# Kernel optimization log

Hardware: AMD Instinct MI355X
Metric: run time of the kernel (lower is better)

Reference implementation:

```python
import jax, jax.numpy as jnp
import numpy as np

N, E, F_IN, F_E, H, HEADS, NG = 50000, 300000, 16, 8, 64, 4, 64
D_HEAD = H // HEADS
EPS = 1e-5


def setup_inputs() -> dict:
    key = jax.random.key(0)
    ks = jax.random.split(key, 12)
    def rn(k, shape, s=0.1):
        return jax.random.normal(k, shape, jnp.float32) * s
    return dict(
        x=jax.random.normal(ks[0], (N, F_IN), jnp.float32),
        edge_index=jax.random.randint(ks[1], (2, E), 0, N),
        edge_attr=jax.random.normal(ks[2], (E, F_E), jnp.float32),
        batch=jnp.sort(jax.random.randint(ks[3], (N,), 0, NG)),
        # edge_net: Linear(F_E, H*F_IN) -> ReLU -> Linear(H*F_IN, H*F_IN)
        en_w1=rn(ks[4], (F_E, H * F_IN)), en_b1=jnp.zeros((H * F_IN,), jnp.float32),
        en_w2=rn(ks[5], (H * F_IN, H * F_IN)), en_b2=jnp.zeros((H * F_IN,), jnp.float32),
        # NNConv root weight + bias
        root_w=rn(ks[6], (F_IN, H)), conv1_b=jnp.zeros((H,), jnp.float32),
        norm1_w=jnp.ones((H,), jnp.float32), norm1_b=jnp.zeros((H,), jnp.float32),
        # GATConv: lin weight, attention vectors, bias
        gat_w=rn(ks[7], (H, H)),
        att_src=rn(ks[8], (HEADS, D_HEAD)), att_dst=rn(ks[9], (HEADS, D_HEAD)),
        gat_b=jnp.zeros((H,), jnp.float32),
        norm2_w=jnp.ones((H,), jnp.float32), norm2_b=jnp.zeros((H,), jnp.float32),
        lin_w=rn(ks[10], (H, 1)), lin_b=jnp.zeros((1,), jnp.float32),
    )


def _graph_layernorm(x, w, b):
    # PyG LayerNorm(mode='graph') with batch=None: scalar mean/std over ALL elems
    mu = x.mean()
    sd = jnp.sqrt(((x - mu) ** 2).mean())
    return (x - mu) / (sd + EPS) * w + b


def reference(x, edge_index, edge_attr, batch, en_w1, en_b1, en_w2, en_b2,
              root_w, conv1_b, norm1_w, norm1_b, gat_w, att_src, att_dst,
              gat_b, norm2_w, norm2_b, lin_w, lin_b):
    src, dst = edge_index[0], edge_index[1]
    # --- NNConv: per-edge weight matrices from edge_net ---
    w_e = jax.nn.relu(edge_attr @ en_w1 + en_b1) @ en_w2 + en_b2
    w_e = w_e.reshape(E, F_IN, H)                      # [E, in, out]
    msg = jnp.einsum('ef,efh->eh', x[src], w_e)        # gather-matmul per edge
    agg = jax.ops.segment_sum(msg, dst, num_segments=N)
    deg = jax.ops.segment_sum(jnp.ones((E,), x.dtype), dst, num_segments=N)
    agg = agg / jnp.maximum(deg, 1.0)[:, None]         # aggr='mean'
    h = x @ root_w + agg + conv1_b
    h = jax.nn.relu(h)
    h = _graph_layernorm(h, norm1_w, norm1_b)
    # dropout: eval mode -> identity
    # --- GATConv (edge_attr=None at call site; add self-loops, softmax attn) ---
    loops = jnp.arange(N)
    s2 = jnp.concatenate([src, loops])
    d2 = jnp.concatenate([dst, loops])
    xh = (h @ gat_w).reshape(N, HEADS, D_HEAD)
    a_src = (xh * att_src).sum(-1)                     # [N, HEADS]
    a_dst = (xh * att_dst).sum(-1)
    alpha = jax.nn.leaky_relu(a_src[s2] + a_dst[d2], 0.2)  # [E+N, HEADS]
    amax = jax.ops.segment_max(alpha, d2, num_segments=N)
    alpha = jnp.exp(alpha - amax[d2])
    asum = jax.ops.segment_sum(alpha, d2, num_segments=N)
    alpha = alpha / (asum[d2] + 1e-16)
    out = jax.ops.segment_sum(alpha[:, :, None] * xh[s2], d2, num_segments=N)
    h2 = out.reshape(N, H) + gat_b                     # concat heads
    h2 = jax.nn.relu(h2)
    h2 = _graph_layernorm(h2, norm2_w, norm2_b)
    # --- global mean pool + linear head ---
    gs = jax.ops.segment_sum(h2, batch, num_segments=NG)
    cnt = jax.ops.segment_sum(jnp.ones((N,), h2.dtype), batch, num_segments=NG)
    pooled = gs / jnp.maximum(cnt, 1.0)[:, None]
    return pooled @ lin_w + lin_b                      # [NG, 1]
```

## Files before the change

kernel.cpp:

```cpp
#include <hip/hip_runtime.h>
#include <hip/hip_bf16.h>

#define N_NODES 50000
#define E_EDGES 300000
#define NGRAPH 64
#define NCHUNK 129
#define CSPLIT 65
#define NKG 1034
#define NEGRP 1172
#define LNEPS 1e-5f
#define NBLK_N 196
#define NBLK_P 12500
#define RPRE16 1.00048828125f

typedef _Float16 f16x8 __attribute__((ext_vector_type(8)));
typedef _Float16 f16x2 __attribute__((ext_vector_type(2)));
typedef float floatx16 __attribute__((ext_vector_type(16)));
typedef float f32x2 __attribute__((ext_vector_type(2)));
typedef unsigned int u32x4 __attribute__((ext_vector_type(4)));

__global__ void k_prep(const float* __restrict__ w2, const float* __restrict__ b2,
                       _Float16* __restrict__ Tt3) {
  __shared__ float tile[32][65];
  int t = threadIdx.x;
  int kg0 = blockIdx.x * 2;
  int kf0 = kg0 * 16;
  int kfr = t >> 6;
  int n0 = t & 63;
#pragma unroll
  for (int it = 0; it < 8; ++it) {
    int kfl = it * 4 + kfr;
    int kf = kf0 + kfl;
    float v = 0.f;
    if (kf < 16384) v = w2[(size_t)kf * 64 + n0];
    else if (kf < 16400) v = b2[(size_t)(kf - 16384) * 64 + n0];
    tile[kfl][n0] = v;
  }
  __syncthreads();
  int kgl = t >> 7;
  int half = (t >> 6) & 1;
  int n = t & 63;
  f16x8 pack;
#pragma unroll
  for (int j = 0; j < 8; ++j) pack[j] = (_Float16)tile[kgl * 16 + half * 8 + j][n];
  *(f16x8*)(Tt3 + (size_t)(kg0 + kgl) * 1024 + half * 512 + n * 8) = pack;
}

__global__ void k_prepw(const float* __restrict__ w1, float* __restrict__ W1t) {
  int i = blockIdx.x * 256 + threadIdx.x;
  if (i < 8192) { int k = i >> 3, j = i & 7; W1t[i] = w1[j * 1024 + k]; }
}

__global__ void k_cnt(const int* __restrict__ ei, int* __restrict__ degI) {
  int e = blockIdx.x * 256 + threadIdx.x;
  if (e < E_EDGES) atomicAdd(&degI[ei[E_EDGES + e]], 1);
}

__global__ void k_scanA(const int* __restrict__ degI, int* __restrict__ bsum) {
  __shared__ int sm[256];
  int t = threadIdx.x;
  int i = blockIdx.x * 256 + t;
  sm[t] = (i < N_NODES) ? degI[i] : 0;
  __syncthreads();
  for (int off = 128; off > 0; off >>= 1) {
    if (t < off) sm[t] += sm[t + off];
    __syncthreads();
  }
  if (t == 0) bsum[blockIdx.x] = sm[0];
}

__global__ void k_scanB(const int* __restrict__ bsum, int* __restrict__ bpre) {
  __shared__ int s[256];
  int t = threadIdx.x;
  int v = (t < NBLK_N) ? bsum[t] : 0;
  s[t] = v;
  __syncthreads();
  for (int off = 1; off < 256; off <<= 1) {
    int add = (t >= off) ? s[t - off] : 0;
    __syncthreads();
    s[t] += add;
    __syncthreads();
  }
  if (t < NBLK_N) bpre[t] = s[t] - v;
}

__global__ void k_scanC(const int* __restrict__ degI, const int* __restrict__ bpre,
                        int* __restrict__ rowptr, int* __restrict__ cursor) {
  __shared__ int s[256];
  int t = threadIdx.x;
  int i = blockIdx.x * 256 + t;
  int d = (i < N_NODES) ? degI[i] : 0;
  s[t] = d;
  __syncthreads();
  for (int off = 1; off < 256; off <<= 1) {
    int add = (t >= off) ? s[t - off] : 0;
    __syncthreads();
    s[t] += add;
    __syncthreads();
  }
  int r = bpre[blockIdx.x] + s[t] - d;
  if (i < N_NODES) {
    rowptr[i] = r;
    cursor[i] = r;
    if (i == N_NODES - 1) rowptr[N_NODES] = r + d;
  }
}

__global__ void k_scatter(const int* __restrict__ ei, int* __restrict__ cursor,
                          int* __restrict__ colsrc) {
  int e = blockIdx.x * 256 + threadIdx.x;
  if (e < E_EDGES) {
    int s = ei[e], d = ei[E_EDGES + e];
    int pos = atomicAdd(&cursor[d], 1);
    colsrc[pos] = s;
  }
}

__global__ __launch_bounds__(256, 4)
void k_nnconv(const float* __restrict__ x, const int* __restrict__ ei,
              const float* __restrict__ ea, const float* __restrict__ W1t,
              const float* __restrict__ b1, const _Float16* __restrict__ Tt3,
              float* __restrict__ agg) {
  const int tid = threadIdx.x;
  const int lane = tid & 63;
  const int l31 = lane & 31;
  const int half = lane >> 5;
  const int grp = blockIdx.x >> 1;
  const int piece = blockIdx.x & 1;
  const int cstart = piece ? CSPLIT : 0;
  const int cend = piece ? NCHUNK : CSPLIT;

  int e = grp * 256 + tid;
  bool valid = e < E_EDGES;
  int srcv = valid ? ei[e] : 0;
  int dstv = valid ? ei[E_EDGES + e] : -1;

  f32x2 ea2[4];
  {
    const float4* p = (const float4*)(ea + (size_t)(valid ? e : 0) * 8);
    float4 a0 = p[0], a1 = p[1];
    ea2[0] = (f32x2){a0.x, a0.y};
    ea2[1] = (f32x2){a0.z, a0.w};
    ea2[2] = (f32x2){a1.x, a1.y};
    ea2[3] = (f32x2){a1.z, a1.w};
  }

  const int f0 = half * 8;
  unsigned xh16[2][4];
#pragma unroll
  for (int mt = 0; mt < 2; ++mt) {
    int s = __shfl(srcv, mt * 32 + l31);
    const float4* px = (const float4*)(x + (size_t)s * 16 + f0);
    float4 v0 = px[0], v1 = px[1];
    xh16[mt][0] = __builtin_bit_cast(unsigned, __builtin_amdgcn_cvt_pkrtz(v0.x * RPRE16, v0.y * RPRE16));
    xh16[mt][1] = __builtin_bit_cast(unsigned, __builtin_amdgcn_cvt_pkrtz(v0.z * RPRE16, v0.w * RPRE16));
    xh16[mt][2] = __builtin_bit_cast(unsigned, __builtin_amdgcn_cvt_pkrtz(v1.x * RPRE16, v1.y * RPRE16));
    xh16[mt][3] = __builtin_bit_cast(unsigned, __builtin_amdgcn_cvt_pkrtz(v1.z * RPRE16, v1.w * RPRE16));
  }

  int bpaddr[2];
#pragma unroll
  for (int mt = 0; mt < 2; ++mt) bpaddr[mt] = (mt * 32 + l31) * 4;

  const _Float16* sb = Tt3 + (size_t)(cstart * 8) * 1024;
  const int loff = half * 512 + l31 * 8;

  f16x8 Bs[4][2];
  auto loadB = [&](int slot) {
    Bs[slot][0] = *(const f16x8*)(sb + loff);
    Bs[slot][1] = *(const f16x8*)(sb + loff + 256);
    sb += 1024;
  };

  unsigned prr[4];
  auto calcR = [&](int c, const float* w1p, const float* b1p) {
    if (c < 128) {
#pragma unroll
      for (int p = 0; p < 4; ++p) {
        float rv[2];
#pragma unroll
        for (int kk = 0; kk < 2; ++kk) {
          const f32x2* w = (const f32x2*)(w1p + (p * 2 + kk) * 8);
          f32x2 s01 = ea2[0] * w[0] + ea2[1] * w[1];
          f32x2 s23 = ea2[2] * w[2] + ea2[3] * w[3];
          f32x2 s = s01 + s23;
          rv[kk] = fmaxf(b1p[p * 2 + kk] + s[0] + s[1], 0.f) * RPRE16;
        }
        prr[p] = __builtin_bit_cast(unsigned, __builtin_amdgcn_cvt_pkrtz(rv[0], rv[1]));
      }
    } else {
      prr[0] = 0x00003C00u;
      prr[1] = prr[2] = prr[3] = 0u;
    }
  };

  unsigned ubuf[8];
  auto bcastR = [&]() {
#pragma unroll
    for (int p = 0; p < 4; ++p)
#pragma unroll
      for (int mt = 0; mt < 2; ++mt)
        ubuf[p * 2 + mt] = (unsigned)__builtin_amdgcn_ds_bpermute(bpaddr[mt], (int)prr[p]);
  };

  floatx16 acc[2][2];
#pragma unroll
  for (int mt = 0; mt < 2; ++mt)
#pragma unroll
    for (int nt = 0; nt < 2; ++nt)
#pragma unroll
      for (int r = 0; r < 16; ++r) acc[mt][nt][r] = 0.f;

  calcR(cstart, W1t + cstart * 64, b1 + cstart * 8);
  bcastR();
  loadB(0);
  loadB(1);
  const float* w1p = W1t + (cstart + 1) * 64;
  const float* b1p = b1 + (cstart + 1) * 8;

  for (int c = cstart; c < cend; ++c) {
    unsigned rsp[16];
#pragma unroll
    for (int p = 0; p < 4; ++p)
#pragma unroll
      for (int mt = 0; mt < 2; ++mt) {
        unsigned u = ubuf[p * 2 + mt];
        rsp[(2 * p) * 2 + mt]     = __builtin_amdgcn_perm(u, 0u, 0x05040504u);
        rsp[(2 * p + 1) * 2 + mt] = __builtin_amdgcn_perm(u, 0u, 0x07060706u);
      }
    if (c + 1 < cend) {
      calcR(c + 1, w1p, b1p);
      bcastR();
      w1p += 64; b1p += 8;
    }
#pragma unroll
    for (int kg = 0; kg < 8; ++kg) {
      loadB((kg + 2) & 3);
#pragma unroll
      for (int mt = 0; mt < 2; ++mt) {
        f16x2 r2 = __builtin_bit_cast(f16x2, rsp[kg * 2 + mt]);
        u32x4 U;
#pragma unroll
        for (int j = 0; j < 4; ++j)
          U[j] = __builtin_bit_cast(unsigned,
                   __builtin_bit_cast(f16x2, xh16[mt][j]) * r2);
        f16x8 A = __builtin_bit_cast(f16x8, U);
#pragma unroll
        for (int nt = 0; nt < 2; ++nt)
          acc[mt][nt] = __builtin_amdgcn_mfma_f32_32x32x16_f16(A, Bs[kg & 3][nt], acc[mt][nt], 0, 0, 0);
      }
    }
  }

#pragma unroll
  for (int mt = 0; mt < 2; ++mt) {
#pragma unroll
    for (int reg = 0; reg < 16; ++reg) {
      int el = mt * 32 + (reg & 3) + 8 * (reg >> 2) + 4 * half;
      int dd = __shfl(dstv, el);
      if (dd >= 0) {
#pragma unroll
        for (int nt = 0; nt < 2; ++nt)
          atomicAdd(&agg[(size_t)dd * 64 + nt * 32 + l31], acc[mt][nt][reg]);
      }
    }
  }
}

__global__ void k_root(const float* __restrict__ x, const float* __restrict__ rootw,
                       const float* __restrict__ conv1b, const float* __restrict__ agg,
                       const int* __restrict__ degI, float* __restrict__ hpre,
                       float* __restrict__ rpart) {
  __shared__ float sW[1024];
  __shared__ float sx[64];
  __shared__ float red[8];
  int t = threadIdx.x;
  int blk = blockIdx.x;
#pragma unroll
  for (int i = 0; i < 4; ++i) sW[t + i * 256] = rootw[t + i * 256];
  if (t < 64) sx[t] = x[(size_t)blk * 64 + t];
  __syncthreads();
  int ln = t >> 6, h = t & 63;
  int n = blk * 4 + ln;
  float acc = conv1b[h];
#pragma unroll
  for (int f = 0; f < 16; ++f) acc += sx[ln * 16 + f] * sW[f * 64 + h];
  float dv = fmaxf((float)degI[n], 1.0f);
  float v = acc + agg[(size_t)n * 64 + h] / dv;
  v = fmaxf(v, 0.f);
  hpre[(size_t)n * 64 + h] = v;
  float s1 = v, s2 = v * v;
  for (int o = 32; o > 0; o >>= 1) { s1 += __shfl_down(s1, o); s2 += __shfl_down(s2, o); }
  if ((t & 63) == 0) { red[t >> 6] = s1; red[4 + (t >> 6)] = s2; }
  __syncthreads();
  if (t == 0) {
    rpart[blk * 2] = red[0] + red[1] + red[2] + red[3];
    rpart[blk * 2 + 1] = red[4] + red[5] + red[6] + red[7];
  }
}

__global__ void k_fold1(const float* __restrict__ rpart, const float* __restrict__ n1w,
                        const float* __restrict__ n1b, const float* __restrict__ gatw,
                        float* __restrict__ gw2, float* __restrict__ tb) {
  __shared__ float red[8];
  __shared__ float sMI[2];
  __shared__ float sS[64], sT[64];
  int t = threadIdx.x;
  int wv = t >> 6, lane = t & 63;
  float a = 0.f, b = 0.f;
  for (int i = t; i < NBLK_P; i += 256) { a += rpart[2 * i]; b += rpart[2 * i + 1]; }
  for (int o = 32; o > 0; o >>= 1) { a += __shfl_down(a, o); b += __shfl_down(b, o); }
  if (lane == 0) { red[wv] = a; red[4 + wv] = b; }
  __syncthreads();
  if (t == 0) {
    float A = red[0] + red[1] + red[2] + red[3];
    float B = red[4] + red[5] + red[6] + red[7];
    const float M = (float)N_NODES * 64.f;
    float mu = A / M;
    float var = fmaxf(B / M - mu * mu, 0.f);
    sMI[0] = mu;
    sMI[1] = 1.f / (sqrtf(var) + LNEPS);
  }
  __syncthreads();
  if (t < 64) {
    float mu = sMI[0], inv = sMI[1];
    sS[t] = inv * n1w[t];
    sT[t] = n1b[t] - mu * inv * n1w[t];
  }
  __syncthreads();
  if (t < 64) {
    float acc = 0.f;
    for (int i = 0; i < 64; ++i) {
      float g = gatw[i * 64 + t];
      gw2[i * 64 + t] = sS[i] * g;
      acc += sT[i] * g;
    }
    tb[t] = acc;
  }
}

__global__ void k_gatlin(const float* __restrict__ hpre, const float* __restrict__ gw2,
                         const float* __restrict__ tb, const float* __restrict__ attS,
                         const float* __restrict__ attD, float* __restrict__ xh,
                         float* __restrict__ asrc, float* __restrict__ adst) {
  __shared__ float sW[4096];
  __shared__ float sh[256];
  __shared__ float sxh[256];
  int t = threadIdx.x;
  int blk = blockIdx.x;
#pragma unroll
  for (int i = 0; i < 16; ++i) sW[t + i * 256] = gw2[t + i * 256];
  sh[t] = hpre[(size_t)blk * 256 + t];
  __syncthreads();
  int ln = t >> 6, h = t & 63;
  float acc = tb[h];
  for (int i = 0; i < 64; ++i) acc += sh[ln * 64 + i] * sW[i * 64 + h];
  xh[(size_t)blk * 256 + t] = acc;
  sxh[t] = acc;
  __syncthreads();
  if (t < 32) {
    int ln2 = t >> 3, rem = t & 7;
    int hd = rem & 3;
    const float* av = (rem >> 2) ? attD : attS;
    float a = 0.f;
#pragma unroll
    for (int d = 0; d < 16; ++d) a += sxh[ln2 * 64 + hd * 16 + d] * av[hd * 16 + d];
    int n = blk * 4 + ln2;
    if (rem >> 2) adst[n * 4 + hd] = a; else asrc[n * 4 + hd] = a;
  }
}

__global__ void k_gat(const int* __restrict__ rowptr, const int* __restrict__ colsrc,
                      const float* __restrict__ xh, const float* __restrict__ asrc,
                      const float* __restrict__ adst, const float* __restrict__ gatb,
                      float* __restrict__ act, float* __restrict__ gpart) {
  __shared__ float sP[4][256];
  __shared__ int sS[4][64];
  __shared__ float sRed[8];
  int t = threadIdx.x;
  int wv = t >> 6, lane = t & 63;
  int n = blockIdx.x * 4 + wv;
  int start = rowptr[n], end = rowptr[n + 1];
  int deg = end - start;
  int myhd = lane >> 4;
  float ad[4];
#pragma unroll
  for (int hd = 0; hd < 4; ++hd) ad[hd] = adst[n * 4 + hd];
  float m[4] = {-1e30f, -1e30f, -1e30f, -1e30f};
  float l[4] = {0.f, 0.f, 0.f, 0.f};
  float O = 0.f;
  int items = deg + 1;
  for (int t0 = 0; t0 < items; t0 += 64) {
    int cnt = min(64, items - t0);
    int idx = t0 + lane;
    bool has = lane < cnt;
    int s = n;
    if (has && idx < deg) s = colsrc[start + idx];
    float a[4];
#pragma unroll
    for (int hd = 0; hd < 4; ++hd) {
      float av = has ? (asrc[s * 4 + hd] + ad[hd]) : -1e30f;
      a[hd] = (av > 0.f) ? av : 0.2f * av;
    }
    float tm[4];
#pragma unroll
    for (int hd = 0; hd < 4; ++hd) tm[hd] = a[hd];
#pragma unroll
    for (int off = 32; off > 0; off >>= 1)
#pragma unroll
      for (int hd = 0; hd < 4; ++hd) tm[hd] = fmaxf(tm[hd], __shfl_xor(tm[hd], off));
    float p[4];
#pragma unroll
    for (int hd = 0; hd < 4; ++hd) {
      float mn = fmaxf(m[hd], tm[hd]);
      float sc = __expf(m[hd] - mn);
      l[hd] *= sc;
      if (hd == myhd) O *= sc;
      m[hd] = mn;
      p[hd] = has ? __expf(a[hd] - mn) : 0.f;
    }
    float ts[4];
#pragma unroll
    for (int hd = 0; hd < 4; ++hd) ts[hd] = p[hd];
#pragma unroll
    for (int off = 32; off > 0; off >>= 1)
#pragma unroll
      for (int hd = 0; hd < 4; ++hd) ts[hd] += __shfl_xor(ts[hd], off);
#pragma unroll
    for (int hd = 0; hd < 4; ++hd) l[hd] += ts[hd];
    sS[wv][lane] = s;
#pragma unroll
    for (int hd = 0; hd < 4; ++hd) sP[wv][lane * 4 + hd] = p[hd];
    for (int e2 = 0; e2 < cnt; ++e2) {
      int ss = sS[wv][e2];
      float pp = sP[wv][e2 * 4 + myhd];
      O = fmaf(pp, xh[(size_t)ss * 64 + lane], O);
    }
  }
  float lmy = (myhd & 2) ? ((myhd & 1) ? l[3] : l[2]) : ((myhd & 1) ? l[1] : l[0]);
  float outv = O / (lmy + 1e-16f);
  float v = fmaxf(outv + gatb[lane], 0.f);
  act[(size_t)n * 64 + lane] = v;
  float s1 = v, s2 = v * v;
#pragma unroll
  for (int off = 32; off > 0; off >>= 1) { s1 += __shfl_down(s1, off); s2 += __shfl_down(s2, off); }
  if (lane == 0) { sRed[wv] = s1; sRed[4 + wv] = s2; }
  __syncthreads();
  if (t == 0) {
    gpart[blockIdx.x * 2] = sRed[0] + sRed[1] + sRed[2] + sRed[3];
    gpart[blockIdx.x * 2 + 1] = sRed[4] + sRed[5] + sRed[6] + sRed[7];
  }
}

__global__ void k_fold2(const float* __restrict__ gpart, const float* __restrict__ n2w,
                        const float* __restrict__ n2b, const float* __restrict__ linw,
                        const float* __restrict__ linb, float* __restrict__ wl) {
  __shared__ float red[8];
  __shared__ float sMI[2];
  int t = threadIdx.x;
  int wv = t >> 6, lane = t & 63;
  float a = 0.f, b = 0.f;
  for (int i = t; i < NBLK_P; i += 256) { a += gpart[2 * i]; b += gpart[2 * i + 1]; }
  for (int o = 32; o > 0; o >>= 1) { a += __shfl_down(a, o); b += __shfl_down(b, o); }
  if (lane == 0) { red[wv] = a; red[4 + wv] = b; }
  __syncthreads();
  if (t == 0) {
    float A = red[0] + red[1] + red[2] + red[3];
    float B = red[4] + red[5] + red[6] + red[7];
    const float M = (float)N_NODES * 64.f;
    float mu = A / M;
    float var = fmaxf(B / M - mu * mu, 0.f);
    sMI[0] = mu;
    sMI[1] = 1.f / (sqrtf(var) + LNEPS);
  }
  __syncthreads();
  if (t < 64) {
    float mu = sMI[0], inv = sMI[1];
    float w = inv * n2w[t] * linw[t];
    float p = (n2b[t] - mu * inv * n2w[t]) * linw[t];
    wl[t] = w;
    for (int o = 32; o > 0; o >>= 1) p += __shfl_down(p, o);
    if (t == 0) wl[64] = p + linb[0];
  }
}

__global__ void k_out(const float* __restrict__ act, const float* __restrict__ wl,
                      const int* __restrict__ batch, float* __restrict__ out) {
  __shared__ float red[4];
  __shared__ float swl[64];
  int g = blockIdx.x;
  int t = threadIdx.x;
  int wv = t >> 6, lane = t & 63;
  if (t < 64) swl[t] = wl[t];
  __syncthreads();
  auto lbound = [&](int key) {
    int lo = 0, hi = N_NODES;
    while (lo < hi) { int mid = (lo + hi) >> 1; if (batch[mid] < key) lo = mid + 1; else hi = mid; }
    return lo;
  };
  int lo = lbound(g), hi = lbound(g + 1);
  int cntn = hi - lo;
  float s = 0.f;
  for (int idx = t; idx < cntn * 64; idx += 256) {
    int n = lo + (idx >> 6);
    int d = idx & 63;
    s += act[(size_t)n * 64 + d] * swl[d];
  }
  for (int o = 32; o > 0; o >>= 1) s += __shfl_down(s, o);
  if (lane == 0) red[wv] = s;
  __syncthreads();
  if (t == 0)
    out[g] = (red[0] + red[1] + red[2] + red[3]) / fmaxf((float)cntn, 1.f) + wl[64];
}

#define OFF_AGG     0UL
#define OFF_DEGI    12800000UL
#define ZBYTES      13000000UL
#define OFF_RPART   13000000UL
#define OFF_GPART   13100032UL
#define OFF_ROWPTR  13200064UL
#define OFF_CURSOR  13400128UL
#define OFF_BSUM    13600192UL
#define OFF_BPRE    13601024UL
#define OFF_COLSRC  13601856UL
#define OFF_TT      14801856UL
#define OFF_W1T     16923584UL
#define OFF_GW2     16956352UL
#define OFF_TB      16972736UL
#define OFF_WL      16972992UL
#define OFF_ASRC    16973312UL
#define OFF_ADST    17773312UL
#define OFF_HPRE    18573312UL
#define OFF_XH      31373312UL
#define OFF_ACT     44173312UL
#define WS_NEED     56973312UL

extern "C" void kernel_launch(void* const* d_in, const int* in_sizes, int n_in,
                              void* d_out, int out_size, void* d_ws, size_t ws_size,
                              hipStream_t stream) {
  const float* x = (const float*)d_in[0];
  const int* ei = (const int*)d_in[1];
  const float* ea = (const float*)d_in[2];
  const int* batch = (const int*)d_in[3];
  const float* w1 = (const float*)d_in[4];
  const float* b1 = (const float*)d_in[5];
  const float* w2 = (const float*)d_in[6];
  const float* b2 = (const float*)d_in[7];
  const float* rootw = (const float*)d_in[8];
  const float* conv1b = (const float*)d_in[9];
  const float* n1w = (const float*)d_in[10];
  const float* n1b = (const float*)d_in[11];
  const float* gatw = (const float*)d_in[12];
  const float* attS = (const float*)d_in[13];
  const float* attD = (const float*)d_in[14];
  const float* gatb = (const float*)d_in[15];
  const float* n2w = (const float*)d_in[16];
  const float* n2b = (const float*)d_in[17];
  const float* linw = (const float*)d_in[18];
  const float* linb = (const float*)d_in[19];

  if (ws_size < WS_NEED) return;
  char* ws = (char*)d_ws;
  float* agg    = (float*)(ws + OFF_AGG);
  int* degI     = (int*)(ws + OFF_DEGI);
  float* rpart  = (float*)(ws + OFF_RPART);
  float* gpart  = (float*)(ws + OFF_GPART);
  int* rowptr   = (int*)(ws + OFF_ROWPTR);
  int* cursor   = (int*)(ws + OFF_CURSOR);
  int* bsum     = (int*)(ws + OFF_BSUM);
  int* bpre     = (int*)(ws + OFF_BPRE);
  int* colsrc   = (int*)(ws + OFF_COLSRC);
  _Float16* Tt3 = (_Float16*)(ws + OFF_TT);
  float* W1t    = (float*)(ws + OFF_W1T);
  float* gw2    = (float*)(ws + OFF_GW2);
  float* tb     = (float*)(ws + OFF_TB);
  float* wl     = (float*)(ws + OFF_WL);
  float* asrc   = (float*)(ws + OFF_ASRC);
  float* adst   = (float*)(ws + OFF_ADST);
  float* hpre   = (float*)(ws + OFF_HPRE);
  float* xh     = (float*)(ws + OFF_XH);
  float* act    = (float*)(ws + OFF_ACT);

  hipMemsetAsync(ws, 0, ZBYTES, stream);

  k_prep<<<(NKG + 1) / 2, 256, 0, stream>>>(w2, b2, Tt3);
  k_prepw<<<32, 256, 0, stream>>>(w1, W1t);
  k_cnt<<<(E_EDGES + 255) / 256, 256, 0, stream>>>(ei, degI);
  k_scanA<<<NBLK_N, 256, 0, stream>>>(degI, bsum);
  k_scanB<<<1, 256, 0, stream>>>(bsum, bpre);
  k_scanC<<<NBLK_N, 256, 0, stream>>>(degI, bpre, rowptr, cursor);
  k_scatter<<<(E_EDGES + 255) / 256, 256, 0, stream>>>(ei, cursor, colsrc);
  k_nnconv<<<NEGRP * 2, 256, 0, stream>>>(x, ei, ea, W1t, b1, Tt3, agg);
  k_root<<<NBLK_P, 256, 0, stream>>>(x, rootw, conv1b, agg, degI, hpre, rpart);
  k_fold1<<<1, 256, 0, stream>>>(rpart, n1w, n1b, gatw, gw2, tb);
  k_gatlin<<<NBLK_P, 256, 0, stream>>>(hpre, gw2, tb, attS, attD, xh, asrc, adst);
  k_gat<<<NBLK_P, 256, 0, stream>>>(rowptr, colsrc, xh, asrc, adst, gatb, act, gpart);
  k_fold2<<<1, 256, 0, stream>>>(gpart, n2w, n2b, linw, linb, wl);
  k_out<<<NGRAPH, 256, 0, stream>>>(act, wl, batch, (float*)d_out);
}
```

Before: 968.5 us.

## Stage edge-net weight tiles into LDS with async global_load_lds double buffering

Result: faster. 914.3 us (-5.6%).

```diff
diff --git a/kernel.cpp b/kernel.cpp
--- a/kernel.cpp
+++ b/kernel.cpp
@@ -19,6 +19,12 @@
 typedef float f32x2 __attribute__((ext_vector_type(2)));
 typedef unsigned int u32x4 __attribute__((ext_vector_type(4)));
 
+__device__ __forceinline__ void async_load16(const void* g, void* l) {
+  __builtin_amdgcn_global_load_lds(
+      (__attribute__((address_space(1))) void*)g,
+      (__attribute__((address_space(3))) void*)l, 16, 0, 0);
+}
+
 __global__ void k_prep(const float* __restrict__ w2, const float* __restrict__ b2,
                        _Float16* __restrict__ Tt3) {
   __shared__ float tile[32][65];
@@ -116,12 +122,14 @@
   }
 }
 
-__global__ __launch_bounds__(256, 4)
+__global__ __launch_bounds__(256, 3)
 void k_nnconv(const float* __restrict__ x, const int* __restrict__ ei,
               const float* __restrict__ ea, const float* __restrict__ W1t,
               const float* __restrict__ b1, const _Float16* __restrict__ Tt3,
               float* __restrict__ agg) {
+  __shared__ __align__(16) _Float16 sB[2][8192];
   const int tid = threadIdx.x;
+  const int wv = tid >> 6;
   const int lane = tid & 63;
   const int l31 = lane & 31;
   const int half = lane >> 5;
@@ -162,14 +170,15 @@
 #pragma unroll
   for (int mt = 0; mt < 2; ++mt) bpaddr[mt] = (mt * 32 + l31) * 4;
 
-  const _Float16* sb = Tt3 + (size_t)(cstart * 8) * 1024;
   const int loff = half * 512 + l31 * 8;
 
-  f16x8 Bs[4][2];
-  auto loadB = [&](int slot) {
-    Bs[slot][0] = *(const f16x8*)(sb + loff);
-    Bs[slot][1] = *(const f16x8*)(sb + loff + 256);
-    sb += 1024;
+  auto stage = [&](int c, int nb) {
+    const _Float16* src = Tt3 + ((size_t)c * 8 + 2 * wv) * 1024 + lane * 8;
+    _Float16* dst = &sB[nb][2 * wv * 1024 + lane * 8];
+    async_load16(src, dst);
+    async_load16(src + 512, dst + 512);
+    async_load16(src + 1024, dst + 1024);
+    async_load16(src + 1536, dst + 1536);
   };
 
   unsigned prr[4];
@@ -213,12 +222,14 @@
 
   calcR(cstart, W1t + cstart * 64, b1 + cstart * 8);
   bcastR();
-  loadB(0);
-  loadB(1);
+  stage(cstart, 0);
+  __syncthreads();
   const float* w1p = W1t + (cstart + 1) * 64;
   const float* b1p = b1 + (cstart + 1) * 8;
 
-  for (int c = cstart; c < cend; ++c) {
+  int c = cstart;
+  int buf = 0;
+  while (true) {
     unsigned rsp[16];
 #pragma unroll
     for (int p = 0; p < 4; ++p)
@@ -228,28 +239,44 @@
         rsp[(2 * p) * 2 + mt]     = __builtin_amdgcn_perm(u, 0u, 0x05040504u);
         rsp[(2 * p + 1) * 2 + mt] = __builtin_amdgcn_perm(u, 0u, 0x07060706u);
       }
-    if (c + 1 < cend) {
+    bool more = (c + 1 < cend);
+    if (more) stage(c + 1, buf ^ 1);
+    if (more) {
       calcR(c + 1, w1p, b1p);
       bcastR();
       w1p += 64; b1p += 8;
     }
-#pragma unroll
-    for (int kg = 0; kg < 8; ++kg) {
-      loadB((kg + 2) & 3);
-#pragma unroll
-      for (int mt = 0; mt < 2; ++mt) {
-        f16x2 r2 = __builtin_bit_cast(f16x2, rsp[kg * 2 + mt]);
-        u32x4 U;
-#pragma unroll
-        for (int j = 0; j < 4; ++j)
-          U[j] = __builtin_bit_cast(unsigned,
-                   __builtin_bit_cast(f16x2, xh16[mt][j]) * r2);
-        f16x8 A = __builtin_bit_cast(f16x8, U);
-#pragma unroll
-        for (int nt = 0; nt < 2; ++nt)
-          acc[mt][nt] = __builtin_amdgcn_mfma_f32_32x32x16_f16(A, Bs[kg & 3][nt], acc[mt][nt], 0, 0, 0);
+    {
+      f16x8 Bs0[2], Bs1[2];
+      Bs0[0] = *(const f16x8*)&sB[buf][loff];
+      Bs0[1] = *(const f16x8*)&sB[buf][loff + 256];
+#pragma unroll
+      for (int kg = 0; kg < 8; ++kg) {
+        f16x8* cur = (kg & 1) ? Bs1 : Bs0;
+        f16x8* nxt = (kg & 1) ? Bs0 : Bs1;
+        if (kg < 7) {
+          nxt[0] = *(const f16x8*)&sB[buf][(kg + 1) * 1024 + loff];
+          nxt[1] = *(const f16x8*)&sB[buf][(kg + 1) * 1024 + loff + 256];
+        }
+#pragma unroll
+        for (int mt = 0; mt < 2; ++mt) {
+          f16x2 r2 = __builtin_bit_cast(f16x2, rsp[kg * 2 + mt]);
+          u32x4 U;
+#pragma unroll
+          for (int j = 0; j < 4; ++j)
+            U[j] = __builtin_bit_cast(unsigned,
+                     __builtin_bit_cast(f16x2, xh16[mt][j]) * r2);
+          f16x8 A = __builtin_bit_cast(f16x8, U);
+#pragma unroll
+          for (int nt = 0; nt < 2; ++nt)
+            acc[mt][nt] = __builtin_amdgcn_mfma_f32_32x32x16_f16(A, cur[nt], acc[mt][nt], 0, 0, 0);
+        }
       }
     }
+    if (!more) break;
+    __syncthreads();
+    buf ^= 1;
+    ++c;
   }
 
 #pragma unroll
```
